# Optimization experiments

Hardware: AMD Instinct MI355X
Metric: run time of the kernel (lower is better)

## Reference

```python
import jax, jax.numpy as jnp
import numpy as np

FP8_MAX = 448.0  # e4m3fn max


def _fake_quant_fp8(x, scale):
    # quantize: scale, clamp, round-trip through float8_e4m3fn; dequantize by 1/scale
    xq = jnp.clip(x * scale, -FP8_MAX, FP8_MAX).astype(jnp.float8_e4m3fn)
    return xq.astype(jnp.float32) * (1.0 / scale)


def _compute_scale(x):
    amax = jnp.max(jnp.abs(x))
    return FP8_MAX / jnp.maximum(amax, 1e-12)


def setup_inputs() -> dict:
    key = jax.random.key(0)
    kx, kw = jax.random.split(key)
    x = jax.random.normal(kx, (8, 2048, 4096), dtype=jnp.float32)
    weight = jax.random.normal(kw, (4096, 4096), dtype=jnp.float32) * 0.02
    return {"x": x, "weight": weight}


def reference(x, weight):
    B, S, K = x.shape
    N = weight.shape[1]
    # weight path: per-tensor scale, fp8 round-trip (transpose in original is value-preserving)
    w_dq = _fake_quant_fp8(weight, _compute_scale(weight))  # [K, N]
    # activation path
    x2d = x.reshape(-1, K)  # [M, K]
    x_dq = _fake_quant_fp8(x2d, _compute_scale(x2d))
    out = x_dq @ w_dq  # fp32 GEMM, [M, N]
    return out.reshape(B, S, N)
```

## Files before the change

### kernel.cpp

```cpp
#include <hip/hip_runtime.h>
#include <stdint.h>

#define FP8_MAX 448.0f

typedef float f32x4 __attribute__((ext_vector_type(4)));
typedef int i32x8 __attribute__((ext_vector_type(8)));
typedef int i32x4 __attribute__((ext_vector_type(4)));

__device__ __forceinline__ unsigned int pack4_fp8(float4 v, float s) {
  float a = fminf(fmaxf(v.x * s, -FP8_MAX), FP8_MAX);
  float b = fminf(fmaxf(v.y * s, -FP8_MAX), FP8_MAX);
  float c = fminf(fmaxf(v.z * s, -FP8_MAX), FP8_MAX);
  float d = fminf(fmaxf(v.w * s, -FP8_MAX), FP8_MAX);
  unsigned int r = (unsigned int)__builtin_amdgcn_cvt_pk_fp8_f32(a, b, 0, false);
  r = (unsigned int)__builtin_amdgcn_cvt_pk_fp8_f32(c, d, (int)r, true);
  return r;
}

__device__ __forceinline__ void load16_to_lds(const void* g, void* l) {
  auto gp = (const __attribute__((address_space(1))) void*)(uintptr_t)g;
  auto lp = (__attribute__((address_space(3))) void*)(unsigned int)(uintptr_t)l;
  __builtin_amdgcn_global_load_lds(gp, lp, 16, 0, 0);
}

__global__ void amax2_kernel(const float* __restrict__ x, int n4x,
                             const float* __restrict__ w, int n4w,
                             unsigned int* __restrict__ hdr) {
  const float4* p4;
  int n4, base, nblk;
  unsigned int* slot;
  if (blockIdx.x < 2048) {
    p4 = (const float4*)x; n4 = n4x; base = blockIdx.x; nblk = 2048; slot = hdr;
  } else {
    p4 = (const float4*)w; n4 = n4w; base = blockIdx.x - 2048; nblk = 512; slot = hdr + 1;
  }
  int i = base * blockDim.x + threadIdx.x;
  int stride = nblk * blockDim.x;
  float m = 0.0f;
  for (; i < n4; i += stride) {
    float4 v = p4[i];
    m = fmaxf(m, fmaxf(fmaxf(fabsf(v.x), fabsf(v.y)), fmaxf(fabsf(v.z), fabsf(v.w))));
  }
#pragma unroll
  for (int off = 32; off > 0; off >>= 1)
    m = fmaxf(m, __shfl_down(m, off, 64));
  __shared__ float wmax[4];
  int lane = threadIdx.x & 63;
  int wv = threadIdx.x >> 6;
  if (lane == 0) wmax[wv] = m;
  __syncthreads();
  if (threadIdx.x == 0) {
    m = fmaxf(fmaxf(wmax[0], wmax[1]), fmaxf(wmax[2], wmax[3]));
    atomicMax(slot, __float_as_uint(m));
  }
}

__global__ void quant_x_kernel(const float* __restrict__ x, unsigned int* __restrict__ xq,
                               const unsigned int* __restrict__ hdr, int n4) {
  float s = FP8_MAX / fmaxf(__uint_as_float(hdr[0]), 1e-12f);
  int i = blockIdx.x * blockDim.x + threadIdx.x;
  int stride = gridDim.x * blockDim.x;
  const float4* x4 = (const float4*)x;
  for (; i < n4; i += stride)
    xq[i] = pack4_fp8(x4[i], s);
}

__global__ void quant_w_t_kernel(const float* __restrict__ w, unsigned char* __restrict__ wqT,
                                 const unsigned int* __restrict__ hdr, int K, int N) {
  __shared__ unsigned int tileT[64][17];
  float s = FP8_MAX / fmaxf(__uint_as_float(hdr[1]), 1e-12f);
  int tk0 = blockIdx.y << 6;
  int tn0 = blockIdx.x << 6;
  int t = threadIdx.x;

  int rn = (t & 15) << 2;
  int rk = (t >> 4) << 2;
  unsigned int wrow[4];
#pragma unroll
  for (int j = 0; j < 4; ++j) {
    float4 v = *(const float4*)(w + (size_t)(tk0 + rk + j) * N + tn0 + rn);
    wrow[j] = pack4_fp8(v, s);
  }
#pragma unroll
  for (int i = 0; i < 4; ++i) {
    unsigned int colw = ((wrow[0] >> (8 * i)) & 0xffu)
                      | (((wrow[1] >> (8 * i)) & 0xffu) << 8)
                      | (((wrow[2] >> (8 * i)) & 0xffu) << 16)
                      | (((wrow[3] >> (8 * i)) & 0xffu) << 24);
    tileT[rn + i][rk >> 2] = colw;
  }
  __syncthreads();

  int n = t >> 2;
  int kc = (t & 3) << 2;
  uint4 v = make_uint4(tileT[n][kc], tileT[n][kc + 1], tileT[n][kc + 2], tileT[n][kc + 3]);
  *(uint4*)(wqT + (size_t)(tn0 + n) * K + tk0 + (kc << 2)) = v;
}

__device__ __forceinline__ i32x8 read_frag(const unsigned char* p, int off0) {
  i32x4 lo = *(const i32x4*)(p + off0);
  i32x4 hi = *(const i32x4*)(p + (off0 ^ 16));
  return __builtin_shufflevector(lo, hi, 0, 1, 2, 3, 4, 5, 6, 7);
}

#define MFMA1(a, b, c) \
  __builtin_amdgcn_mfma_scale_f32_16x16x128_f8f6f4(a, b, c, 0, 0, 0, 0x7f7f7f7f, 0, 0x7f7f7f7f)

#define MFMA_Q(M0_, N0_)                                              \
  do {                                                                \
    __builtin_amdgcn_s_setprio(1);                                    \
    acc[M0_ + 0][N0_ + 0] = MFMA1(af[0], bf[N0_ + 0], acc[M0_ + 0][N0_ + 0]); \
    acc[M0_ + 0][N0_ + 1] = MFMA1(af[0], bf[N0_ + 1], acc[M0_ + 0][N0_ + 1]); \
    acc[M0_ + 1][N0_ + 0] = MFMA1(af[1], bf[N0_ + 0], acc[M0_ + 1][N0_ + 0]); \
    acc[M0_ + 1][N0_ + 1] = MFMA1(af[1], bf[N0_ + 1], acc[M0_ + 1][N0_ + 1]); \
    acc[M0_ + 2][N0_ + 0] = MFMA1(af[2], bf[N0_ + 0], acc[M0_ + 2][N0_ + 0]); \
    acc[M0_ + 2][N0_ + 1] = MFMA1(af[2], bf[N0_ + 1], acc[M0_ + 2][N0_ + 1]); \
    acc[M0_ + 3][N0_ + 0] = MFMA1(af[3], bf[N0_ + 0], acc[M0_ + 3][N0_ + 0]); \
    acc[M0_ + 3][N0_ + 1] = MFMA1(af[3], bf[N0_ + 1], acc[M0_ + 3][N0_ + 1]); \
    __builtin_amdgcn_s_setprio(0);                                    \
  } while (0)

#define BAR() __builtin_amdgcn_s_barrier()
#define LGKM0()                                           \
  do {                                                    \
    asm volatile("s_waitcnt lgkmcnt(0)" ::: "memory");    \
    __builtin_amdgcn_sched_barrier(0);                    \
  } while (0)
#define VMCNT(N_)                                               \
  do {                                                          \
    asm volatile("s_waitcnt vmcnt(" #N_ ")" ::: "memory");      \
    __builtin_amdgcn_sched_barrier(0);                          \
  } while (0)

__global__ __launch_bounds__(512, 2) void gemm_fp8_kernel(
    const unsigned char* __restrict__ Aq,
    const unsigned char* __restrict__ Bq,
    const unsigned int* __restrict__ hdr,
    float* __restrict__ out, int M, int N, int K) {
  __shared__ __align__(16) unsigned char smem[131072];

  const int t = threadIdx.x;
  const int wave = t >> 6;
  const int lane = t & 63;
  const int row16 = lane & 15;
  const int quad = lane >> 4;
  const int wr = wave >> 2;
  const int wc = wave & 3;
  const int m0 = blockIdx.y << 8;
  const int n0 = blockIdx.x << 8;

  const int sRow = (wave << 3) + (lane >> 3);
  const int sCol = (((lane & 7) ^ (lane >> 3)) << 4);
  const unsigned char* agBase = Aq + (size_t)(m0 + sRow) * K + sCol;
  const unsigned char* bgBase = Bq + (size_t)(n0 + sRow) * K + sCol;
  const int ldsStageOff = (wave << 10) + (lane << 4);

  auto stageA = [&](int u, int h) {
    const int buf = (u & 1) << 15;
#pragma unroll
    for (int r = 0; r < 2; ++r)
      load16_to_lds(agBase + (size_t)((h << 7) + (r << 6)) * K + ((size_t)u << 7),
                    smem + buf + (h << 14) + (r << 13) + ldsStageOff);
  };
  auto stageB = [&](int u, int h) {
    const int buf = (u & 1) << 15;
#pragma unroll
    for (int r = 0; r < 2; ++r)
      load16_to_lds(bgBase + (size_t)((h << 7) + (r << 6)) * K + ((size_t)u << 7),
                    smem + 65536 + buf + (h << 14) + (r << 13) + ldsStageOff);
  };

  const int off0 = (((quad << 1) ^ (row16 & 7)) << 4);
  const int aRow = (wr << 7) + row16;
  const int bRow = (wc << 6) + row16;

  f32x4 acc[8][4] = {};

  const int NT = K >> 7;

  stageA(0, 0); stageA(0, 1); stageB(0, 0); stageB(0, 1);
  stageA(1, 0); stageB(1, 0);
  VMCNT(4);
  BAR();

  auto tile_body = [&](int tt, bool stg1, bool stg2, int waitN) {
    const int buf = (tt & 1) << 15;
    const unsigned char* Ab = smem + buf;
    const unsigned char* Bb = smem + 65536 + buf;
    i32x8 af[4], bf[4];
    af[0] = read_frag(Ab + ((aRow + 0) << 7), off0);
    af[1] = read_frag(Ab + ((aRow + 16) << 7), off0);
    af[2] = read_frag(Ab + ((aRow + 32) << 7), off0);
    af[3] = read_frag(Ab + ((aRow + 48) << 7), off0);
    bf[0] = read_frag(Bb + ((bRow + 0) << 7), off0);
    bf[1] = read_frag(Bb + ((bRow + 16) << 7), off0);
    if (stg1) stageA(tt + 1, 1);
    BAR();
    LGKM0();
    MFMA_Q(0, 0);
    BAR();
    bf[2] = read_frag(Bb + ((bRow + 32) << 7), off0);
    bf[3] = read_frag(Bb + ((bRow + 48) << 7), off0);
    if (stg1) stageB(tt + 1, 1);
    BAR();
    LGKM0();
    MFMA_Q(0, 2);
    BAR();
    af[0] = read_frag(Ab + ((aRow + 64) << 7), off0);
    af[1] = read_frag(Ab + ((aRow + 80) << 7), off0);
    af[2] = read_frag(Ab + ((aRow + 96) << 7), off0);
    af[3] = read_frag(Ab + ((aRow + 112) << 7), off0);
    if (stg2) stageB(tt + 2, 0);
    BAR();
    LGKM0();
    MFMA_Q(4, 0);
    BAR();
    if (stg2) stageA(tt + 2, 0);
    if (waitN == 4) {
      VMCNT(4);
    } else if (waitN == 0) {
      VMCNT(0);
    }
    BAR();
    MFMA_Q(4, 2);
    BAR();
  };

  for (int tt = 0; tt < NT - 2; ++tt) tile_body(tt, true, true, 4);
  tile_body(NT - 2, true, false, 0);
  tile_body(NT - 1, false, false, -1);

  const float ax = fmaxf(__uint_as_float(hdr[0]), 1e-12f);
  const float aw = fmaxf(__uint_as_float(hdr[1]), 1e-12f);
  const float sc = (ax / FP8_MAX) * (aw / FP8_MAX);
#pragma unroll
  for (int mi = 0; mi < 8; ++mi) {
#pragma unroll
    for (int ni = 0; ni < 4; ++ni) {
      const int gc = n0 + (wc << 6) + ni * 16 + row16;
#pragma unroll
      for (int r = 0; r < 4; ++r) {
        const int gr = m0 + (wr << 7) + mi * 16 + quad * 4 + r;
        out[(size_t)gr * N + gc] = acc[mi][ni][r] * sc;
      }
    }
  }
}

extern "C" void kernel_launch(void* const* d_in, const int* in_sizes, int n_in,
                              void* d_out, int out_size, void* d_ws, size_t ws_size,
                              hipStream_t stream) {
  const float* x = (const float*)d_in[0];
  const float* w = (const float*)d_in[1];
  float* out = (float*)d_out;

  const int K = 4096;
  const int N = 4096;
  const int M = in_sizes[0] / K;

  unsigned int* hdr = (unsigned int*)d_ws;
  unsigned char* xq = (unsigned char*)d_ws + 16;
  unsigned char* wqT = xq + (size_t)M * K;

  hipMemsetAsync(d_ws, 0, 16, stream);

  amax2_kernel<<<2560, 256, 0, stream>>>(x, (int)((size_t)M * K / 4), w,
                                         (int)((size_t)K * N / 4), hdr);

  quant_x_kernel<<<4096, 256, 0, stream>>>(x, (unsigned int*)xq, hdr, (int)((size_t)M * K / 4));
  quant_w_t_kernel<<<dim3(N / 64, K / 64), 256, 0, stream>>>(w, wqT, hdr, K, N);

  gemm_fp8_kernel<<<dim3(N / 256, M / 256), 512, 0, stream>>>(xq, wqT, hdr, out, M, N, K);
}
```

Measured before the change: 808.9 us.

## Double-buffer LDS fragment registers and prefetch next tile during last MFMA quad

Splits the A/B fragment registers into two sets, issues all LDS fragment reads for the second half of the tile up front, and uses partial lgkmcnt waits so that each MFMA quad waits only for the fragments it needs. The first-half fragments of the next tile are prefetched from the other LDS buffer while the final MFMA quad runs. The aim is to hide LDS read latency behind matrix instructions instead of stalling on lgkmcnt(0) before each quad. In exchange it needs more VGPRs, which could hurt occupancy at launch bounds 512x2, and correctness depends on the lgkmcnt counts matching the order in which the reads and LDS-direct loads are issued.

Result: slower. 832.8 us (+3.0%).

```diff
diff --git a/kernel.cpp b/kernel.cpp
--- a/kernel.cpp
+++ b/kernel.cpp
@@ -106,25 +106,26 @@
 #define MFMA1(a, b, c) \
   __builtin_amdgcn_mfma_scale_f32_16x16x128_f8f6f4(a, b, c, 0, 0, 0, 0x7f7f7f7f, 0, 0x7f7f7f7f)
 
-#define MFMA_Q(M0_, N0_)                                              \
-  do {                                                                \
-    __builtin_amdgcn_s_setprio(1);                                    \
-    acc[M0_ + 0][N0_ + 0] = MFMA1(af[0], bf[N0_ + 0], acc[M0_ + 0][N0_ + 0]); \
-    acc[M0_ + 0][N0_ + 1] = MFMA1(af[0], bf[N0_ + 1], acc[M0_ + 0][N0_ + 1]); \
-    acc[M0_ + 1][N0_ + 0] = MFMA1(af[1], bf[N0_ + 0], acc[M0_ + 1][N0_ + 0]); \
-    acc[M0_ + 1][N0_ + 1] = MFMA1(af[1], bf[N0_ + 1], acc[M0_ + 1][N0_ + 1]); \
-    acc[M0_ + 2][N0_ + 0] = MFMA1(af[2], bf[N0_ + 0], acc[M0_ + 2][N0_ + 0]); \
-    acc[M0_ + 2][N0_ + 1] = MFMA1(af[2], bf[N0_ + 1], acc[M0_ + 2][N0_ + 1]); \
-    acc[M0_ + 3][N0_ + 0] = MFMA1(af[3], bf[N0_ + 0], acc[M0_ + 3][N0_ + 0]); \
-    acc[M0_ + 3][N0_ + 1] = MFMA1(af[3], bf[N0_ + 1], acc[M0_ + 3][N0_ + 1]); \
-    __builtin_amdgcn_s_setprio(0);                                    \
+#define MFMA_Q(AF_, BF_, M0_, N0_)                                          \
+  do {                                                                      \
+    __builtin_amdgcn_s_setprio(1);                                          \
+    acc[M0_ + 0][N0_ + 0] = MFMA1(AF_[0], BF_[0], acc[M0_ + 0][N0_ + 0]);   \
+    acc[M0_ + 0][N0_ + 1] = MFMA1(AF_[0], BF_[1], acc[M0_ + 0][N0_ + 1]);   \
+    acc[M0_ + 1][N0_ + 0] = MFMA1(AF_[1], BF_[0], acc[M0_ + 1][N0_ + 0]);   \
+    acc[M0_ + 1][N0_ + 1] = MFMA1(AF_[1], BF_[1], acc[M0_ + 1][N0_ + 1]);   \
+    acc[M0_ + 2][N0_ + 0] = MFMA1(AF_[2], BF_[0], acc[M0_ + 2][N0_ + 0]);   \
+    acc[M0_ + 2][N0_ + 1] = MFMA1(AF_[2], BF_[1], acc[M0_ + 2][N0_ + 1]);   \
+    acc[M0_ + 3][N0_ + 0] = MFMA1(AF_[3], BF_[0], acc[M0_ + 3][N0_ + 0]);   \
+    acc[M0_ + 3][N0_ + 1] = MFMA1(AF_[3], BF_[1], acc[M0_ + 3][N0_ + 1]);   \
+    __builtin_amdgcn_s_setprio(0);                                          \
   } while (0)
 
 #define BAR() __builtin_amdgcn_s_barrier()
-#define LGKM0()                                           \
-  do {                                                    \
-    asm volatile("s_waitcnt lgkmcnt(0)" ::: "memory");    \
-    __builtin_amdgcn_sched_barrier(0);                    \
+#define SCHED0() __builtin_amdgcn_sched_barrier(0)
+#define LGKMC(N_)                                              \
+  do {                                                         \
+    asm volatile("s_waitcnt lgkmcnt(" #N_ ")" ::: "memory");   \
+    __builtin_amdgcn_sched_barrier(0);                         \
   } while (0)
 #define VMCNT(N_)                                               \
   do {                                                          \
@@ -175,45 +176,45 @@
   const int bRow = (wc << 6) + row16;
 
   f32x4 acc[8][4] = {};
+  i32x8 afA[4], afB[4], bfA[2], bfB[2];
 
   const int NT = K >> 7;
 
   stageA(0, 0); stageA(0, 1); stageB(0, 0); stageB(0, 1);
-  stageA(1, 0); stageB(1, 0);
+  stageB(1, 0); stageA(1, 0);
   VMCNT(4);
   BAR();
-
-  auto tile_body = [&](int tt, bool stg1, bool stg2, int waitN) {
+#pragma unroll
+  for (int i = 0; i < 4; ++i)
+    afA[i] = read_frag(smem + ((aRow + i * 16) << 7), off0);
+  bfA[0] = read_frag(smem + 65536 + ((bRow + 0) << 7), off0);
+  bfA[1] = read_frag(smem + 65536 + ((bRow + 16) << 7), off0);
+
+  auto tile_body = [&](int tt, bool stg1, bool stg2, int waitN, bool pref) {
     const int buf = (tt & 1) << 15;
     const unsigned char* Ab = smem + buf;
     const unsigned char* Bb = smem + 65536 + buf;
-    i32x8 af[4], bf[4];
-    af[0] = read_frag(Ab + ((aRow + 0) << 7), off0);
-    af[1] = read_frag(Ab + ((aRow + 16) << 7), off0);
-    af[2] = read_frag(Ab + ((aRow + 32) << 7), off0);
-    af[3] = read_frag(Ab + ((aRow + 48) << 7), off0);
-    bf[0] = read_frag(Bb + ((bRow + 0) << 7), off0);
-    bf[1] = read_frag(Bb + ((bRow + 16) << 7), off0);
+    bfB[0] = read_frag(Bb + ((bRow + 32) << 7), off0);
+    bfB[1] = read_frag(Bb + ((bRow + 48) << 7), off0);
+    SCHED0();
+    afB[0] = read_frag(Ab + ((aRow + 64) << 7), off0);
+    afB[1] = read_frag(Ab + ((aRow + 80) << 7), off0);
+    afB[2] = read_frag(Ab + ((aRow + 96) << 7), off0);
+    afB[3] = read_frag(Ab + ((aRow + 112) << 7), off0);
     if (stg1) stageA(tt + 1, 1);
     BAR();
-    LGKM0();
-    MFMA_Q(0, 0);
-    BAR();
-    bf[2] = read_frag(Bb + ((bRow + 32) << 7), off0);
-    bf[3] = read_frag(Bb + ((bRow + 48) << 7), off0);
+    LGKMC(12);
+    MFMA_Q(afA, bfA, 0, 0);
+    BAR();
     if (stg1) stageB(tt + 1, 1);
     BAR();
-    LGKM0();
-    MFMA_Q(0, 2);
-    BAR();
-    af[0] = read_frag(Ab + ((aRow + 64) << 7), off0);
-    af[1] = read_frag(Ab + ((aRow + 80) << 7), off0);
-    af[2] = read_frag(Ab + ((aRow + 96) << 7), off0);
-    af[3] = read_frag(Ab + ((aRow + 112) << 7), off0);
+    LGKMC(8);
+    MFMA_Q(afA, bfB, 0, 2);
+    BAR();
     if (stg2) stageB(tt + 2, 0);
     BAR();
-    LGKM0();
-    MFMA_Q(4, 0);
+    LGKMC(0);
+    MFMA_Q(afB, bfA, 4, 0);
     BAR();
     if (stg2) stageA(tt + 2, 0);
     if (waitN == 4) {
@@ -222,13 +223,23 @@
       VMCNT(0);
     }
     BAR();
-    MFMA_Q(4, 2);
+    if (pref) {
+      const unsigned char* An = smem + (buf ^ 32768);
+      const unsigned char* Bn = smem + 65536 + (buf ^ 32768);
+      afA[0] = read_frag(An + ((aRow + 0) << 7), off0);
+      afA[1] = read_frag(An + ((aRow + 16) << 7), off0);
+      afA[2] = read_frag(An + ((aRow + 32) << 7), off0);
+      afA[3] = read_frag(An + ((aRow + 48) << 7), off0);
+      bfA[0] = read_frag(Bn + ((bRow + 0) << 7), off0);
+      bfA[1] = read_frag(Bn + ((bRow + 16) << 7), off0);
+    }
+    MFMA_Q(afB, bfB, 4, 2);
     BAR();
   };
 
-  for (int tt = 0; tt < NT - 2; ++tt) tile_body(tt, true, true, 4);
-  tile_body(NT - 2, true, false, 0);
-  tile_body(NT - 1, false, false, -1);
+  for (int tt = 0; tt < NT - 2; ++tt) tile_body(tt, true, true, 4, true);
+  tile_body(NT - 2, true, false, 0, true);
+  tile_body(NT - 1, false, false, -1, false);
 
   const float ax = fmaxf(__uint_as_float(hdr[0]), 1e-12f);
   const float aw = fmaxf(__uint_as_float(hdr[1]), 1e-12f);
```
